# Kernel tuning notes

Hardware: AMD Instinct MI355X
Metric: run time of the kernel (lower is better)

## Reference

```python
import jax, jax.numpy as jnp
import numpy as np

N_USERS = 100000
N_ITEMS = 50000
EMB_DIM = 64
N_EDGES = 1000000
N_HOPS = 3
EPS = 1e-12  # F.normalize default eps


def _l2_normalize(x):
    # F.normalize(x): x / max(||x||_2, eps) along dim=1
    norm = jnp.sqrt(jnp.sum(x * x, axis=1, keepdims=True))
    return x / jnp.maximum(norm, EPS)


def setup_inputs() -> dict:
    key = jax.random.key(0)
    k1, k2, k3, k4 = jax.random.split(key, 4)
    user_emb = jax.random.normal(k1, (N_USERS, EMB_DIM), dtype=jnp.float32)
    item_emb = jax.random.normal(k2, (N_ITEMS, EMB_DIM), dtype=jnp.float32)
    user_indices = jax.random.randint(k3, (N_EDGES,), 0, N_USERS, dtype=jnp.int32)
    item_indices = jax.random.randint(k4, (N_EDGES,), 0, N_ITEMS, dtype=jnp.int32)
    return {"user_emb": user_emb, "item_emb": item_emb,
            "user_indices": user_indices, "item_indices": item_indices}


def reference(user_emb, item_emb, user_indices, item_indices):
    # mess_dropout=False, node_dropout=False (deterministic reference)
    user_agg = user_emb
    item_agg = item_emb
    user_ui_emb = jnp.zeros_like(user_emb)
    item_ui_emb = jnp.zeros_like(item_emb)
    for _ in range(N_HOPS):
        # bipartite message passing: gather from opposite side, scatter_add to own side
        msg_to_users = item_agg[item_indices]            # [E, D]
        msg_to_items = user_agg[user_indices]            # [E, D]
        user_agg = jax.ops.segment_sum(msg_to_users, user_indices, num_segments=N_USERS)
        item_agg = jax.ops.segment_sum(msg_to_items, item_indices, num_segments=N_ITEMS)
        item_agg = _l2_normalize(item_agg)
        user_agg = _l2_normalize(user_agg)
        user_ui_emb = user_agg + user_ui_emb
        item_ui_emb = item_agg + item_ui_emb
    item_ui_emb = item_ui_emb + item_emb
    user_ui_emb = user_ui_emb + user_emb
    return (item_ui_emb, user_ui_emb)
```

## Files before the change

kernel.cpp:

```cpp
#include <hip/hip_runtime.h>

#define N_USERS 100000
#define N_ITEMS 50000
#define NROWS (N_USERS + N_ITEMS)
#define EMB 64
#define N_EDGES 1000000

#define SH_U 9
#define SH_I 8
#define NBUK 196
#define B1 256
#define CHUNK ((N_EDGES + B1 - 1) / B1)
#define HN (2 * NBUK * B1)
#define HTILE 4096
#define HTILES ((HN + HTILE - 1) / HTILE)
#define DBINS 64

typedef unsigned short u16;
typedef u16 us8 __attribute__((ext_vector_type(8)));
typedef u16 us4 __attribute__((ext_vector_type(4)));
typedef float f4 __attribute__((ext_vector_type(4)));

static __device__ __forceinline__ float bf2f(u16 h) {
    return __uint_as_float(((unsigned)h) << 16);
}
static __device__ __forceinline__ u16 f2bf(float f) {
    unsigned u = __float_as_uint(f);
    return (u16)((u + 0x7FFFu + ((u >> 16) & 1u)) >> 16);
}

static __device__ __forceinline__ int hphys(int L) {
    int sb = L >> 8;
    int blk = L & 255;
    return blk * (2 * NBUK) + sb;
}

__global__ void conv_kernel(const float* __restrict__ a, u16* __restrict__ b, int n4) {
    int t = blockIdx.x * blockDim.x + threadIdx.x;
    if (t >= n4) return;
    f4 v = ((const f4*)a)[t];
    us4 w;
    w.x = f2bf(v.x); w.y = f2bf(v.y); w.z = f2bf(v.z); w.w = f2bf(v.w);
    ((us4*)b)[t] = w;
}

__global__ void histA_kernel(const int* __restrict__ uidx, const int* __restrict__ iidx,
                             int* __restrict__ H) {
    __shared__ int hu[NBUK];
    __shared__ int hi[NBUK];
    int tid = threadIdx.x, blk = blockIdx.x;
    for (int b = tid; b < NBUK; b += 256) { hu[b] = 0; hi[b] = 0; }
    __syncthreads();
    int e0 = blk * CHUNK;
    int e1 = e0 + CHUNK; if (e1 > N_EDGES) e1 = N_EDGES;
    for (int e = e0 + tid; e < e1; e += 256) {
        atomicAdd(&hu[uidx[e] >> SH_U], 1);
        atomicAdd(&hi[iidx[e] >> SH_I], 1);
    }
    __syncthreads();
    int* Hb = H + blk * (2 * NBUK);
    for (int b = tid; b < NBUK; b += 256) {
        Hb[b] = hu[b];
        Hb[NBUK + b] = hi[b];
    }
}

__global__ void hscan_tile_kernel(const int* __restrict__ H, int* __restrict__ part) {
    int t = blockIdx.x, tid = threadIdx.x;
    int base = t * HTILE;
    int s = 0;
    for (int i = tid; i < HTILE; i += 256) {
        int L = base + i;
        if (L < HN) s += H[hphys(L)];
    }
    #pragma unroll
    for (int o = 32; o > 0; o >>= 1) s += __shfl_xor(s, o);
    __shared__ int wsum[4];
    if ((tid & 63) == 0) wsum[tid >> 6] = s;
    __syncthreads();
    if (tid == 0) part[t] = wsum[0] + wsum[1] + wsum[2] + wsum[3];
}

__global__ void hscan_write_kernel(const int* __restrict__ H, const int* __restrict__ part,
                                   int* __restrict__ HB) {
    int t = blockIdx.x, tid = threadIdx.x;
    int base = t * HTILE;

    __shared__ int lds[HTILE];
    for (int i = tid; i < HTILE; i += 256) {
        int L = base + i;
        lds[i] = (L < HN) ? H[hphys(L)] : 0;
    }
    __syncthreads();

    int pbase = 0;
    for (int p = 0; p < t; ++p) pbase += part[p];

    int tsum = 0;
    #pragma unroll
    for (int i = 0; i < 16; ++i) tsum += lds[tid * 16 + i];

    int lane = tid & 63, wid = tid >> 6;
    int x = tsum;
    #pragma unroll
    for (int o = 1; o < 64; o <<= 1) {
        int tt = __shfl_up(x, o);
        if (lane >= o) x += tt;
    }
    __shared__ int wsum[4];
    if (lane == 63) wsum[wid] = x;
    __syncthreads();
    int wbase = 0;
    for (int w = 0; w < wid; ++w) wbase += wsum[w];

    int run = pbase + wbase + x - tsum;
    #pragma unroll
    for (int i = 0; i < 16; ++i) {
        int L = base + tid * 16 + i;
        if (L < HN) HB[L] = run;
        run += lds[tid * 16 + i];
    }
}

__global__ void scatterA_kernel(const int* __restrict__ uidx, const int* __restrict__ iidx,
                                const int* __restrict__ HB, int* __restrict__ rec) {
    __shared__ int cu[NBUK];
    __shared__ int ci[NBUK];
    int tid = threadIdx.x, blk = blockIdx.x;
    for (int sb = tid; sb < 2 * NBUK; sb += 256) {
        int v = HB[sb * B1 + blk];
        if (sb < NBUK) cu[sb] = v; else ci[sb - NBUK] = v;
    }
    __syncthreads();
    int e0 = blk * CHUNK;
    int e1 = e0 + CHUNK; if (e1 > N_EDGES) e1 = N_EDGES;
    for (int e = e0 + tid; e < e1; e += 256) {
        int u = uidx[e];
        int i = iidx[e];
        int pu = atomicAdd(&cu[u >> SH_U], 1);
        rec[pu] = ((u & 511) << 16) | i;
        int pi = atomicAdd(&ci[i >> SH_I], 1);
        rec[pi] = ((i & 255) << 17) | u;
    }
}

__global__ void bucketB_kernel(const int* __restrict__ HB, const int* __restrict__ rec,
                               int* __restrict__ offs_u, int* __restrict__ offs_i,
                               int* __restrict__ list) {
    int sb = blockIdx.x, tid = threadIdx.x;
    int side = (sb >= NBUK) ? 1 : 0;
    int b = sb - side * NBUK;
    int start = HB[sb * B1];
    int end = (sb == 2 * NBUK - 1) ? 2 * N_EDGES : HB[(sb + 1) * B1];
    int shift = side ? 17 : 16;
    int mask  = side ? 0x1FFFF : 0xFFFF;
    int nd    = side ? 256 : 512;
    int dbase = side ? (b << SH_I) : (b << SH_U);
    int n     = side ? N_ITEMS : N_USERS;
    int rel   = start - side * N_EDGES;
    int* offs = side ? offs_i : offs_u;

    __shared__ int cnt[512];
    __shared__ int scn[512];
    __shared__ int wsum[4];
    if (tid < 256) { cnt[tid] = 0; cnt[256 + tid] = 0; }
    __syncthreads();

    for (int r = start + tid; r < end; r += 256)
        atomicAdd(&cnt[rec[r] >> shift], 1);
    __syncthreads();

    int a0 = cnt[2 * tid], a1 = cnt[2 * tid + 1];
    int s = a0 + a1;
    int lane = tid & 63, wid = tid >> 6;
    int x = s;
    #pragma unroll
    for (int o = 1; o < 64; o <<= 1) {
        int tt = __shfl_up(x, o);
        if (lane >= o) x += tt;
    }
    if (lane == 63) wsum[wid] = x;
    __syncthreads();
    int wbase = 0;
    for (int w = 0; w < wid; ++w) wbase += wsum[w];
    int excl = wbase + x - s;
    scn[2 * tid] = excl;
    scn[2 * tid + 1] = excl + a0;
    __syncthreads();

    for (int dl = tid; dl < nd; dl += 256) {
        int dg = dbase + dl;
        if (dg < n) offs[dg] = rel + scn[dl];
    }
    if (b == NBUK - 1 && tid == 0) offs[n] = (end - side * N_EDGES);
    __syncthreads();

    for (int r = start + tid; r < end; r += 256) {
        int v = rec[r];
        int dl = v >> shift;
        int pos = atomicAdd(&scn[dl], 1);
        list[start + pos] = (v & mask) << 7;
    }
}

static __device__ __forceinline__ int row_degree(const int* offs_u, const int* offs_i, int r) {
    int d = (r < N_USERS) ? (offs_u[r + 1] - offs_u[r])
                          : (offs_i[r - N_USERS + 1] - offs_i[r - N_USERS]);
    return (d > DBINS - 1) ? DBINS - 1 : d;
}

__global__ void deg_hist_kernel(const int* __restrict__ offs_u, const int* __restrict__ offs_i,
                                int* __restrict__ dhist) {
    __shared__ int h[DBINS];
    int tid = threadIdx.x;
    if (tid < DBINS) h[tid] = 0;
    __syncthreads();
    int r = blockIdx.x * 256 + tid;
    if (r < NROWS) atomicAdd(&h[row_degree(offs_u, offs_i, r)], 1);
    __syncthreads();
    if (tid < DBINS && h[tid]) atomicAdd(&dhist[tid], h[tid]);
}

__global__ void deg_scan_kernel(const int* __restrict__ dhist, int* __restrict__ dcur) {
    int lane = threadIdx.x;
    int v = dhist[lane];
    int x = v;
    #pragma unroll
    for (int o = 1; o < 64; o <<= 1) {
        int tt = __shfl_up(x, o);
        if (lane >= o) x += tt;
    }
    dcur[lane] = x - v;
}

__global__ void deg_build_kernel(const int* __restrict__ offs_u, const int* __restrict__ offs_i,
                                 int* __restrict__ dcur, int* __restrict__ perm) {
    __shared__ int h[DBINS];
    __shared__ int base[DBINS];
    int tid = threadIdx.x;
    if (tid < DBINS) h[tid] = 0;
    __syncthreads();
    int r = blockIdx.x * 256 + tid;
    int d = -1;
    if (r < NROWS) {
        d = row_degree(offs_u, offs_i, r);
        atomicAdd(&h[d], 1);
    }
    __syncthreads();
    if (tid < DBINS) {
        base[tid] = h[tid] ? atomicAdd(&dcur[tid], h[tid]) : 0;
        h[tid] = 0;
    }
    __syncthreads();
    if (r < NROWS) {
        int p = atomicAdd(&h[d], 1);
        perm[base[d] + p] = r;
    }
}

__global__ void gather_norm_v3(const u16* __restrict__ srcU,
                               const u16* __restrict__ srcI,
                               const int* __restrict__ offs_u, const int* __restrict__ list_u,
                               const int* __restrict__ offs_i, const int* __restrict__ list_i,
                               const int* __restrict__ perm,
                               u16* __restrict__ aggU, u16* __restrict__ aggI,
                               const u16* __restrict__ h0U, const u16* __restrict__ h0I,
                               const u16* __restrict__ h1U, const u16* __restrict__ h1I,
                               float* __restrict__ outU, float* __restrict__ outI,
                               const float* __restrict__ initU, const float* __restrict__ initI,
                               int final_hop) {
    int t = blockIdx.x * blockDim.x + threadIdx.x;
    int lane = t & 63;
    int grp = lane >> 3, sub = lane & 7;
    int slot = (t >> 6) * 8 + grp;

    int rid = (slot < NROWS) ? perm[slot] : -1;
    bool valid = rid >= 0;
    bool isU = valid && (rid < N_USERS);
    int rr = isU ? rid : rid - N_USERS;

    int beg = 0, deg = 0;
    if (valid) {
        const int* offs = isU ? offs_u : offs_i;
        beg = offs[rr];
        deg = offs[rr + 1] - beg;
    }
    const int* list = isU ? list_u : list_i;
    const u16* src  = isU ? srcU : srcI;
    const char* srcB = (const char*)src;
    unsigned suboff = (unsigned)(sub << 4);
    const int* lp = list + beg;

    int dmax = deg;
    dmax = max(dmax, __shfl_xor(dmax, 8));
    dmax = max(dmax, __shfl_xor(dmax, 16));
    dmax = max(dmax, __shfl_xor(dmax, 32));

    float acc[8] = {0.f, 0.f, 0.f, 0.f, 0.f, 0.f, 0.f, 0.f};

    #pragma unroll 4
    for (int e = 0; e < dmax; ++e) {
        if (e < deg) {
            unsigned jb = (unsigned)lp[e];
            us8 v = *(const us8*)(srcB + (jb + suboff));
            #pragma unroll
            for (int i = 0; i < 8; ++i) acc[i] += bf2f(v[i]);
        }
    }

    float q = 0.f;
    #pragma unroll
    for (int i = 0; i < 8; ++i) q += acc[i] * acc[i];
    q += __shfl_xor(q, 1);
    q += __shfl_xor(q, 2);
    q += __shfl_xor(q, 4);
    float inv = 1.f / fmaxf(sqrtf(q), 1e-12f);

    if (!valid) return;
    size_t ro = (size_t)rr * EMB + (sub << 3);

    if (!final_hop) {
        u16* agg = isU ? aggU : aggI;
        us8 w;
        #pragma unroll
        for (int i = 0; i < 8; ++i) w[i] = f2bf(acc[i] * inv);
        *(us8*)(agg + ro) = w;
    } else {
        const u16* h0 = isU ? h0U : h0I;
        const u16* h1 = isU ? h1U : h1I;
        const float* init = isU ? initU : initI;
        float* out = isU ? outU : outI;
        us8 a = *(const us8*)(h0 + ro);
        us8 b = *(const us8*)(h1 + ro);
        f4 i0 = *(const f4*)(init + ro);
        f4 i1 = *(const f4*)(init + ro + 4);
        f4 r0, r1;
        r0.x = i0.x + bf2f(a[0]) + bf2f(b[0]) + acc[0] * inv;
        r0.y = i0.y + bf2f(a[1]) + bf2f(b[1]) + acc[1] * inv;
        r0.z = i0.z + bf2f(a[2]) + bf2f(b[2]) + acc[2] * inv;
        r0.w = i0.w + bf2f(a[3]) + bf2f(b[3]) + acc[3] * inv;
        r1.x = i1.x + bf2f(a[4]) + bf2f(b[4]) + acc[4] * inv;
        r1.y = i1.y + bf2f(a[5]) + bf2f(b[5]) + acc[5] * inv;
        r1.z = i1.z + bf2f(a[6]) + bf2f(b[6]) + acc[6] * inv;
        r1.w = i1.w + bf2f(a[7]) + bf2f(b[7]) + acc[7] * inv;
        *(f4*)(out + ro)     = r0;
        *(f4*)(out + ro + 4) = r1;
    }
}

extern "C" void kernel_launch(void* const* d_in, const int* in_sizes, int n_in,
                              void* d_out, int out_size, void* d_ws, size_t ws_size,
                              hipStream_t stream) {
    const float* user_emb = (const float*)d_in[0];
    const float* item_emb = (const float*)d_in[1];
    const int*   uidx     = (const int*)d_in[2];
    const int*   iidx     = (const int*)d_in[3];

    float* out      = (float*)d_out;
    float* out_item = out;
    float* out_user = out + (size_t)N_ITEMS * EMB;

    u16* ws16    = (u16*)d_ws;
    u16* ua_bf   = ws16;
    u16* ub_bf   = ua_bf + (size_t)N_USERS * EMB;
    u16* ia_bf   = ub_bf + (size_t)N_USERS * EMB;
    u16* ib_bf   = ia_bf + (size_t)N_ITEMS * EMB;
    u16* uemb_bf = ib_bf + (size_t)N_ITEMS * EMB;
    u16* iemb_bf = uemb_bf + (size_t)N_USERS * EMB;
    int* rec     = (int*)(iemb_bf + (size_t)N_ITEMS * EMB);
    int* list    = rec + 2 * N_EDGES;
    int* list_u  = list;
    int* list_i  = list + N_EDGES;
    int* offs_u  = list + 2 * N_EDGES;
    int* offs_i  = offs_u + (N_USERS + 1);
    int* H       = offs_i + (N_ITEMS + 1);
    int* HB      = H + HN;
    int* part    = HB + HN;
    int* dhist   = part + HTILES;
    int* dcur    = dhist + DBINS;
    int* perm    = dcur + DBINS;

    conv_kernel<<<(N_USERS * EMB / 4 + 255) / 256, 256, 0, stream>>>(user_emb, uemb_bf, N_USERS * EMB / 4);
    conv_kernel<<<(N_ITEMS * EMB / 4 + 255) / 256, 256, 0, stream>>>(item_emb, iemb_bf, N_ITEMS * EMB / 4);

    histA_kernel<<<B1, 256, 0, stream>>>(uidx, iidx, H);
    hscan_tile_kernel<<<HTILES, 256, 0, stream>>>(H, part);
    hscan_write_kernel<<<HTILES, 256, 0, stream>>>(H, part, HB);
    scatterA_kernel<<<B1, 256, 0, stream>>>(uidx, iidx, HB, rec);
    bucketB_kernel<<<2 * NBUK, 256, 0, stream>>>(HB, rec, offs_u, offs_i, list);

    hipMemsetAsync(dhist, 0, DBINS * sizeof(int), stream);
    int dblocks = (NROWS + 255) / 256;
    deg_hist_kernel<<<dblocks, 256, 0, stream>>>(offs_u, offs_i, dhist);
    deg_scan_kernel<<<1, 64, 0, stream>>>(dhist, dcur);
    deg_build_kernel<<<dblocks, 256, 0, stream>>>(offs_u, offs_i, dcur, perm);

    const int gthreads = ((NROWS + 7) / 8) * 64;
    const int gblocks = (gthreads + 255) / 256;

    gather_norm_v3<<<gblocks, 256, 0, stream>>>(
        iemb_bf, uemb_bf, offs_u, list_u, offs_i, list_i, perm,
        ua_bf, ia_bf, nullptr, nullptr, nullptr, nullptr,
        nullptr, nullptr, nullptr, nullptr, 0);

    gather_norm_v3<<<gblocks, 256, 0, stream>>>(
        ia_bf, ua_bf, offs_u, list_u, offs_i, list_i, perm,
        ub_bf, ib_bf, nullptr, nullptr, nullptr, nullptr,
        nullptr, nullptr, nullptr, nullptr, 0);

    gather_norm_v3<<<gblocks, 256, 0, stream>>>(
        ib_bf, ub_bf, offs_u, list_u, offs_i, list_i, perm,
        nullptr, nullptr, ua_bf, ia_bf, ub_bf, ib_bf,
        out_user, out_item, user_emb, item_emb, 1);
}
```

Baseline: 258.5 us.

## Fuse degree-sorted row permutation into bucket kernel with local per-bucket sort

After: 239.2 us. 1.08x faster.

```diff
diff --git a/kernel.cpp b/kernel.cpp
--- a/kernel.cpp
+++ b/kernel.cpp
@@ -146,7 +146,7 @@
 
 __global__ void bucketB_kernel(const int* __restrict__ HB, const int* __restrict__ rec,
                                int* __restrict__ offs_u, int* __restrict__ offs_i,
-                               int* __restrict__ list) {
+                               int* __restrict__ list, int* __restrict__ perm) {
     int sb = blockIdx.x, tid = threadIdx.x;
     int side = (sb >= NBUK) ? 1 : 0;
     int b = sb - side * NBUK;
@@ -163,7 +163,10 @@
     __shared__ int cnt[512];
     __shared__ int scn[512];
     __shared__ int wsum[4];
+    __shared__ int dh[DBINS];
+    __shared__ int dsc[DBINS];
     if (tid < 256) { cnt[tid] = 0; cnt[256 + tid] = 0; }
+    if (tid < DBINS) dh[tid] = 0;
     __syncthreads();
 
     for (int r = start + tid; r < end; r += 256)
@@ -201,60 +204,31 @@
         int pos = atomicAdd(&scn[dl], 1);
         list[start + pos] = (v & mask) << 7;
     }
-}
-
-static __device__ __forceinline__ int row_degree(const int* offs_u, const int* offs_i, int r) {
-    int d = (r < N_USERS) ? (offs_u[r + 1] - offs_u[r])
-                          : (offs_i[r - N_USERS + 1] - offs_i[r - N_USERS]);
-    return (d > DBINS - 1) ? DBINS - 1 : d;
-}
-
-__global__ void deg_hist_kernel(const int* __restrict__ offs_u, const int* __restrict__ offs_i,
-                                int* __restrict__ dhist) {
-    __shared__ int h[DBINS];
-    int tid = threadIdx.x;
-    if (tid < DBINS) h[tid] = 0;
-    __syncthreads();
-    int r = blockIdx.x * 256 + tid;
-    if (r < NROWS) atomicAdd(&h[row_degree(offs_u, offs_i, r)], 1);
-    __syncthreads();
-    if (tid < DBINS && h[tid]) atomicAdd(&dhist[tid], h[tid]);
-}
-
-__global__ void deg_scan_kernel(const int* __restrict__ dhist, int* __restrict__ dcur) {
-    int lane = threadIdx.x;
-    int v = dhist[lane];
-    int x = v;
-    #pragma unroll
-    for (int o = 1; o < 64; o <<= 1) {
-        int tt = __shfl_up(x, o);
-        if (lane >= o) x += tt;
-    }
-    dcur[lane] = x - v;
-}
-
-__global__ void deg_build_kernel(const int* __restrict__ offs_u, const int* __restrict__ offs_i,
-                                 int* __restrict__ dcur, int* __restrict__ perm) {
-    __shared__ int h[DBINS];
-    __shared__ int base[DBINS];
-    int tid = threadIdx.x;
-    if (tid < DBINS) h[tid] = 0;
-    __syncthreads();
-    int r = blockIdx.x * 256 + tid;
-    int d = -1;
-    if (r < NROWS) {
-        d = row_degree(offs_u, offs_i, r);
-        atomicAdd(&h[d], 1);
+
+    int nv = n - dbase; if (nv > nd) nv = nd;
+    for (int dl = tid; dl < nv; dl += 256) {
+        int d = cnt[dl]; if (d > DBINS - 1) d = DBINS - 1;
+        atomicAdd(&dh[d], 1);
     }
     __syncthreads();
     if (tid < DBINS) {
-        base[tid] = h[tid] ? atomicAdd(&dcur[tid], h[tid]) : 0;
-        h[tid] = 0;
-    }
-    __syncthreads();
-    if (r < NROWS) {
-        int p = atomicAdd(&h[d], 1);
-        perm[base[d] + p] = r;
+        int v = dh[tid];
+        int xx = v;
+        #pragma unroll
+        for (int o = 1; o < DBINS; o <<= 1) {
+            int tt = __shfl_up(xx, o);
+            if (tid >= o) xx += tt;
+        }
+        dsc[tid] = xx - v;
+    }
+    __syncthreads();
+    if (tid < DBINS) dh[tid] = dsc[tid];
+    __syncthreads();
+    int pwbase = side ? (N_USERS + dbase) : dbase;
+    for (int dl = tid; dl < nv; dl += 256) {
+        int d = cnt[dl]; if (d > DBINS - 1) d = DBINS - 1;
+        int p = atomicAdd(&dh[d], 1);
+        perm[pwbase + p] = pwbase + dl;
     }
 }
 
@@ -298,7 +272,7 @@
 
     float acc[8] = {0.f, 0.f, 0.f, 0.f, 0.f, 0.f, 0.f, 0.f};
 
-    #pragma unroll 4
+    #pragma unroll 8
     for (int e = 0; e < dmax; ++e) {
         if (e < deg) {
             unsigned jb = (unsigned)lp[e];
@@ -376,9 +350,7 @@
     int* H       = offs_i + (N_ITEMS + 1);
     int* HB      = H + HN;
     int* part    = HB + HN;
-    int* dhist   = part + HTILES;
-    int* dcur    = dhist + DBINS;
-    int* perm    = dcur + DBINS;
+    int* perm    = part + HTILES;
 
     conv_kernel<<<(N_USERS * EMB / 4 + 255) / 256, 256, 0, stream>>>(user_emb, uemb_bf, N_USERS * EMB / 4);
     conv_kernel<<<(N_ITEMS * EMB / 4 + 255) / 256, 256, 0, stream>>>(item_emb, iemb_bf, N_ITEMS * EMB / 4);
@@ -387,13 +359,7 @@
     hscan_tile_kernel<<<HTILES, 256, 0, stream>>>(H, part);
     hscan_write_kernel<<<HTILES, 256, 0, stream>>>(H, part, HB);
     scatterA_kernel<<<B1, 256, 0, stream>>>(uidx, iidx, HB, rec);
-    bucketB_kernel<<<2 * NBUK, 256, 0, stream>>>(HB, rec, offs_u, offs_i, list);
-
-    hipMemsetAsync(dhist, 0, DBINS * sizeof(int), stream);
-    int dblocks = (NROWS + 255) / 256;
-    deg_hist_kernel<<<dblocks, 256, 0, stream>>>(offs_u, offs_i, dhist);
-    deg_scan_kernel<<<1, 64, 0, stream>>>(dhist, dcur);
-    deg_build_kernel<<<dblocks, 256, 0, stream>>>(offs_u, offs_i, dcur, perm);
+    bucketB_kernel<<<2 * NBUK, 256, 0, stream>>>(HB, rec, offs_u, offs_i, list, perm);
 
     const int gthreads = ((NROWS + 7) / 8) * 64;
     const int gblocks = (gthreads + 255) / 256;
```
